# Kernel tuning notes

Hardware: AMD Instinct MI355X
Metric: run time of the kernel (lower is better)

## Reference

```python
import jax, jax.numpy as jnp
import numpy as np

N_ATOMS = 10000
N_EDGES = 160000
N_SPECIES = 8
N_STRUCT = 8
C = 16        # n_element_channels
N_MAX = 4     # radial functions per l
N_BASIS = 8   # bessel basis size
L_MAX = 3
CUTOFF = 5.0
K = N_MAX * C             # equivariant channels per l (k_max_l)
K_TOTAL = (L_MAX + 1) * K  # concatenated invariants


def _sph_harm(u):
    """Real spherical harmonics l=0..3 for unit vectors u [E,3] -> [E,16]."""
    x, y, z = u[:, 0], u[:, 1], u[:, 2]
    x2, y2, z2 = x * x, y * y, z * z
    one = jnp.ones_like(x)
    ys = [
        0.28209479 * one,
        0.48860251 * y, 0.48860251 * z, 0.48860251 * x,
        1.09254843 * x * y, 1.09254843 * y * z,
        0.31539157 * (3.0 * z2 - 1.0),
        1.09254843 * x * z, 0.54627422 * (x2 - y2),
        0.59004359 * y * (3.0 * x2 - y2), 2.89061144 * x * y * z,
        0.45704579 * y * (5.0 * z2 - 1.0), 0.37317633 * z * (5.0 * z2 - 3.0),
        0.45704579 * x * (5.0 * z2 - 1.0), 1.44530572 * z * (x2 - y2),
        0.59004359 * x * (x2 - 3.0 * y2),
    ]
    return jnp.stack(ys, axis=-1)


def _radial(r, W_rad):
    """Bessel radial basis with cosine cutoff, projected per l. r [E] -> [E, L+1, N_MAX]."""
    n = jnp.arange(1, N_BASIS + 1, dtype=r.dtype)
    rr = jnp.maximum(r, 1e-6)
    basis = jnp.sqrt(2.0 / CUTOFF) * jnp.sin(n[None, :] * jnp.pi * rr[:, None] / CUTOFF) / rr[:, None]
    fc = 0.5 * (jnp.cos(jnp.pi * jnp.clip(r / CUTOFF, 0.0, 1.0)) + 1.0)  # smooth cutoff
    return jnp.einsum('eb,lbn->eln', basis * fc[:, None], W_rad)


def _mp_layer(h, senders, receivers, sh, R, W_inv, cemb):
    """One equivariant message-passing + CG(l x l -> 0) invariant contraction."""
    hs = h[senders]  # gather neighbor scalars [E, C]
    invs = []
    for l in range(L_MAX + 1):
        sl = sh[:, l * l:(l + 1) * (l + 1)]  # [E, 2l+1]
        # edge message: sh x radial x neighbor features -> [E, 2l+1, N_MAX*C]
        M = jnp.einsum('em,en,ec->emnc', sl, R[:, l], hs)
        M = M.reshape(M.shape[0], 2 * l + 1, K)
        A = jax.ops.segment_sum(M, receivers, num_segments=N_ATOMS)  # scatter to centers
        # CG l (x) l -> L=0 invariant (real-SH convention)
        invs.append(jnp.einsum('nmk,nmk->nk', A, A) / jnp.sqrt(2.0 * l + 1.0))
    inv = jnp.concatenate(invs, axis=-1)  # [N, K_TOTAL]
    h_new = (inv @ W_inv) * cemb  # center element embedding
    return h_new, inv


def setup_inputs() -> dict:
    key = jax.random.key(0)
    ks = jax.random.split(key, 10)
    positions = jax.random.uniform(ks[0], (N_ATOMS, 3), jnp.float32, 0.0, 3.0)
    senders = jax.random.randint(ks[1], (N_EDGES,), 0, N_ATOMS)
    receivers = jax.random.randint(ks[2], (N_EDGES,), 0, N_ATOMS)
    species = jax.random.randint(ks[3], (N_ATOMS,), 0, N_SPECIES)
    structure_ids = jnp.sort(jax.random.randint(ks[4], (N_ATOMS,), 0, N_STRUCT))
    embed = jax.random.normal(ks[5], (N_SPECIES, C), jnp.float32)
    W_rad = jax.random.normal(ks[6], (L_MAX + 1, N_BASIS, N_MAX), jnp.float32) * 0.3
    W_inv1 = jax.random.normal(ks[7], (K_TOTAL, C), jnp.float32) / np.sqrt(K_TOTAL)
    W_inv2 = jax.random.normal(ks[8], (K_TOTAL, C), jnp.float32) / np.sqrt(K_TOTAL)
    w_out = jax.random.normal(ks[9], (K_TOTAL,), jnp.float32) / np.sqrt(K_TOTAL)
    comp_weights = jnp.zeros((N_SPECIES,), jnp.float32)
    return {"positions": positions, "embed": embed, "W_rad": W_rad,
            "W_inv1": W_inv1, "W_inv2": W_inv2, "w_out": w_out,
            "comp_weights": comp_weights, "senders": senders,
            "receivers": receivers, "species": species,
            "structure_ids": structure_ids}


def reference(positions, embed, W_rad, W_inv1, W_inv2, w_out, comp_weights,
              senders, receivers, species, structure_ids):
    rvec = positions[receivers] - positions[senders]          # [E,3]
    r = jnp.linalg.norm(rvec, axis=-1)
    u = rvec / jnp.maximum(r, 1e-6)[:, None]
    sh = _sph_harm(u)                                          # [E,16]
    R = _radial(r, W_rad)                                      # [E,4,N_MAX]
    cemb = embed[species]                                      # center embedding [N,C]
    h = cemb                                                   # initial features
    h, _ = _mp_layer(h, senders, receivers, sh, R, W_inv1, cemb)
    h, inv2 = _mp_layer(h, senders, receivers, sh, R, W_inv2, cemb)
    e_atom = inv2 @ w_out + comp_weights[species]              # per-atom energies [N]
    return jax.ops.segment_sum(e_atom, structure_ids, num_segments=N_STRUCT)
```

## Files before the change

kernel.cpp:

```cpp
#include <hip/hip_runtime.h>

#define N_ATOMS 10000
#define N_EDGES 160000
#define N_STRUCT 8
#define D_PAD 48
#define EDW 48
#define N_SLOTS (N_ATOMS * D_PAD)
#define B4 4
#define PI_F 3.14159265358979323846f


__global__ void init_kernel(int* __restrict__ cursor, float* __restrict__ accum) {
    int i = blockIdx.x * blockDim.x + threadIdx.x;
    if (i < N_ATOMS) cursor[i] = i * D_PAD;
    if (i < N_STRUCT) accum[i] = 0.f;
}

__global__ void scatter_kernel(const int* __restrict__ receivers, int* __restrict__ cursor,
                               int* __restrict__ perm) {
    int e = blockIdx.x * blockDim.x + threadIdx.x;
    if (e < N_EDGES) perm[e] = atomicAdd(&cursor[receivers[e]], 1);
}

__global__ void pad_kernel(const int* __restrict__ cursor, float* __restrict__ edat) {
    int i = blockIdx.x * blockDim.x + threadIdx.x;
    if (i >= N_ATOMS * 3) return;
    int a = i / 3, j = i % 3;
    int cnt = cursor[a] - a * D_PAD;
    if (cnt > D_PAD) cnt = D_PAD;
    int c4 = (cnt + B4 - 1) / B4 * B4;
    if (c4 > D_PAD) c4 = D_PAD;
    int slot = cnt + j;
    if (slot < c4) {
        float4 z = make_float4(0.f, 0.f, 0.f, 0.f);
        float4* p = (float4*)(edat + (size_t)(a * D_PAD + slot) * EDW);
        #pragma unroll
        for (int k = 0; k < 12; ++k) p[k] = z;
    }
}

__global__ void emb_kernel(const float* __restrict__ embed, const int* __restrict__ species,
                           float* __restrict__ h0) {
    int i = blockIdx.x * blockDim.x + threadIdx.x;
    if (i < N_ATOMS * 16) {
        int a = i >> 4, c = i & 15;
        h0[i] = embed[species[a] * 16 + c];
    }
}

__global__ void gather_hs(const int* __restrict__ snd, const int* __restrict__ cursor,
                          const float* __restrict__ h, float* __restrict__ edat) {
    int slot = blockIdx.x * blockDim.x + threadIdx.x;
    if (slot >= N_SLOTS) return;
    int a = slot / D_PAD, j = slot - a * D_PAD;
    int cnt = cursor[a] - a * D_PAD;
    if (cnt > D_PAD) cnt = D_PAD;
    if (j >= cnt) return;
    int s = snd[slot];
    const float4* hp = (const float4*)(h + (size_t)s * 16);
    float4* ep = (float4*)(edat + (size_t)slot * EDW + 32);
    ep[0] = hp[0]; ep[1] = hp[1]; ep[2] = hp[2]; ep[3] = hp[3];
}

__global__ void transpose_winv(const float* __restrict__ A, const float* __restrict__ B,
                               float* __restrict__ AT, float* __restrict__ BT) {
    int i = blockIdx.x * blockDim.x + threadIdx.x;
    if (i < 4096) {
        int k = i >> 4, c = i & 15;
        AT[c * 256 + k] = A[i];
    } else if (i < 8192) {
        int j = i - 4096;
        int k = j >> 4, c = j & 15;
        BT[c * 256 + k] = B[j];
    }
}


__global__ void edge_geom(const float* __restrict__ pos, const float* __restrict__ W_rad,
                          const int* __restrict__ senders, const int* __restrict__ receivers,
                          const int* __restrict__ perm,
                          float* __restrict__ edat, int* __restrict__ snd) {
    int e = blockIdx.x * blockDim.x + threadIdx.x;
    if (e >= N_EDGES) return;
    int s = senders[e], rc = receivers[e];
    int p = perm[e];
    float dx = pos[rc * 3 + 0] - pos[s * 3 + 0];
    float dy = pos[rc * 3 + 1] - pos[s * 3 + 1];
    float dz = pos[rc * 3 + 2] - pos[s * 3 + 2];
    float r = sqrtf(dx * dx + dy * dy + dz * dz);
    float rr = fmaxf(r, 1e-6f);
    float inv = 1.0f / rr;
    float x = dx * inv, y = dy * inv, z = dz * inv;
    float x2 = x * x, y2 = y * y, z2 = z * z;
    float she[16];
    she[0]  = 0.28209479f;
    she[1]  = 0.48860251f * y;
    she[2]  = 0.48860251f * z;
    she[3]  = 0.48860251f * x;
    she[4]  = 1.09254843f * x * y;
    she[5]  = 1.09254843f * y * z;
    she[6]  = 0.31539157f * (3.0f * z2 - 1.0f);
    she[7]  = 1.09254843f * x * z;
    she[8]  = 0.54627422f * (x2 - y2);
    she[9]  = 0.59004359f * y * (3.0f * x2 - y2);
    she[10] = 2.89061144f * x * y * z;
    she[11] = 0.45704579f * y * (5.0f * z2 - 1.0f);
    she[12] = 0.37317633f * z * (5.0f * z2 - 3.0f);
    she[13] = 0.45704579f * x * (5.0f * z2 - 1.0f);
    she[14] = 1.44530572f * z * (x2 - y2);
    she[15] = 0.59004359f * x * (x2 - 3.0f * y2);
    float* ed = edat + (size_t)p * EDW;
    ((float4*)ed)[0] = make_float4(she[0], she[1], she[2], she[3]);
    ((float4*)ed)[1] = make_float4(she[4], she[5], she[6], she[7]);
    ((float4*)ed)[2] = make_float4(she[8], she[9], she[10], she[11]);
    ((float4*)ed)[3] = make_float4(she[12], she[13], she[14], she[15]);
    float fc = 0.5f * (cosf(PI_F * fminf(r * 0.2f, 1.0f)) + 1.0f);
    const float c0 = 0.6324555320336759f;
    float bfv[8];
    #pragma unroll
    for (int n = 0; n < 8; ++n)
        bfv[n] = c0 * sinf((float)(n + 1) * PI_F * rr * 0.2f) * inv * fc;
    float Re[16];
    #pragma unroll
    for (int l = 0; l < 4; ++l) {
        #pragma unroll
        for (int n = 0; n < 4; ++n) {
            float acc = 0.0f;
            #pragma unroll
            for (int b = 0; b < 8; ++b) acc = fmaf(bfv[b], W_rad[l * 32 + b * 4 + n], acc);
            Re[l * 4 + n] = acc;
        }
    }
    ((float4*)ed)[4] = make_float4(Re[0], Re[1], Re[2], Re[3]);
    ((float4*)ed)[5] = make_float4(Re[4], Re[5], Re[6], Re[7]);
    ((float4*)ed)[6] = make_float4(Re[8], Re[9], Re[10], Re[11]);
    ((float4*)ed)[7] = make_float4(Re[12], Re[13], Re[14], Re[15]);
    snd[p] = s;
}


__global__ __launch_bounds__(64, 7) void mp_accum(
    const float* __restrict__ edat,
    const int* __restrict__ cursor,
    float* __restrict__ Abuf)
{
    const int lane = threadIdx.x;
    const int atom = blockIdx.x;
    const int m = lane >> 2, cg = lane & 3;
    const int l = (m >= 9) ? 3 : (m >= 4) ? 2 : (m >= 1) ? 1 : 0;
    const int l4 = l * 4, cg4 = cg * 4;

    int cnt = cursor[atom] - atom * D_PAD;
    if (cnt > D_PAD) cnt = D_PAD;
    const int nb = (cnt + B4 - 1) / B4;

    const float* strip = edat + (size_t)atom * (D_PAD * EDW);

    float acc[4][4];
    #pragma unroll
    for (int n = 0; n < 4; ++n)
        #pragma unroll
        for (int j = 0; j < 4; ++j) acc[n][j] = 0.f;

    for (int b = 0; b < nb; ++b) {
        const float* bp = strip + b * (B4 * EDW);
        float  shv[B4];
        float4 rv[B4];
        float4 hv[B4];
        #pragma unroll
        for (int q = 0; q < B4; ++q) {
            const float* eq = bp + q * EDW;
            shv[q] = eq[m];
            rv[q]  = *(const float4*)(eq + 16 + l4);
            hv[q]  = *(const float4*)(eq + 32 + cg4);
        }
        #pragma unroll
        for (int q = 0; q < B4; ++q) {
            float hvj[4] = {hv[q].x, hv[q].y, hv[q].z, hv[q].w};
            float rvn[4] = {rv[q].x, rv[q].y, rv[q].z, rv[q].w};
            #pragma unroll
            for (int j = 0; j < 4; ++j) {
                float ww = shv[q] * hvj[j];
                #pragma unroll
                for (int n = 0; n < 4; ++n)
                    acc[n][j] = fmaf(ww, rvn[n], acc[n][j]);
            }
        }
    }

    float* Ap = Abuf + (size_t)atom * 1024 + m * 64 + cg4;
    #pragma unroll
    for (int n = 0; n < 4; ++n)
        *(float4*)&Ap[n * 16] =
            make_float4(acc[n][0], acc[n][1], acc[n][2], acc[n][3]);
}


#define SROW 260

__global__ __launch_bounds__(256, 2) void mp_inv2(
    const float* __restrict__ Abuf,
    const float* __restrict__ W_invT,
    const float* __restrict__ cemb, float* __restrict__ h_out,
    const float* __restrict__ w_out, const float* __restrict__ comp_w,
    const int* __restrict__ species, const int* __restrict__ sids,
    float* __restrict__ accum, int do_energy)
{
    __shared__ __attribute__((aligned(16))) float sWT[16 * SROW];
    __shared__ __attribute__((aligned(16))) float sInv[16 * SROW];
    __shared__ __attribute__((aligned(16))) float sTmp[4][1024];
    __shared__ float sE[16];

    const int t = threadIdx.x;
    const int w = t >> 6, lane = t & 63;
    const int blk = blockIdx.x;

    if (!do_energy) {
        #pragma unroll
        for (int i = 0; i < 16; ++i) {
            int idx = i * 256 + t;
            sWT[(idx >> 8) * SROW + (idx & 255)] = W_invT[idx];
        }
    }

    const float4* A4 = (const float4*)Abuf;
    #pragma unroll
    for (int g = 0; g < 4; ++g) {
        const int atomL = g * 4 + w;
        const int atom = blk * 16 + atomL;
        #pragma unroll
        for (int i = 0; i < 4; ++i) {
            float4 v = A4[(size_t)atom * 256 + i * 64 + lane];
            *(float4*)&sTmp[w][(i * 64 + lane) * 4] =
                make_float4(v.x * v.x, v.y * v.y, v.z * v.z, v.w * v.w);
        }
        const float* T = &sTmp[w][0];
        const int k = lane;
        float s0 = T[k];
        float s1 = T[64 + k] + T[128 + k] + T[192 + k];
        float s2 = T[256 + k] + T[320 + k] + T[384 + k] + T[448 + k] + T[512 + k];
        float s3 = T[576 + k] + T[640 + k] + T[704 + k] + T[768 + k]
                 + T[832 + k] + T[896 + k] + T[960 + k];
        const float i0 = s0;
        const float i1 = s1 * 0.57735026918962576f;
        const float i2 = s2 * 0.44721359549995794f;
        const float i3 = s3 * 0.37796447300922720f;

        if (do_energy) {
            float pe = i0 * w_out[k] + i1 * w_out[64 + k]
                     + i2 * w_out[128 + k] + i3 * w_out[192 + k];
            #pragma unroll
            for (int off = 32; off > 0; off >>= 1) pe += __shfl_down(pe, off);
            if (lane == 0) sE[atomL] = pe;
        } else {
            float* si = &sInv[atomL * SROW];
            si[k] = i0; si[64 + k] = i1; si[128 + k] = i2; si[192 + k] = i3;
        }
    }
    __syncthreads();

    if (do_energy) {
        if (t == 0) {
            const int base = blk * 16;
            int cursid = sids[base];
            float run = 0.f;
            for (int a = 0; a < 16; ++a) {
                int sid = sids[base + a];
                float e = sE[a] + comp_w[species[base + a]];
                if (sid != cursid) { atomicAdd(&accum[cursid], run); run = 0.f; cursid = sid; }
                run += e;
            }
            atomicAdd(&accum[cursid], run);
        }
    } else {
        const int aL = t >> 4, c = t & 15;
        const float* ivp = &sInv[aL * SROW];
        const float* wvp = &sWT[c * SROW];
        float p = 0.f;
        #pragma unroll
        for (int kk = 0; kk < 64; ++kk) {
            float4 iv = *(const float4*)&ivp[kk * 4];
            float4 wv = *(const float4*)&wvp[kk * 4];
            p = fmaf(iv.x, wv.x, p);
            p = fmaf(iv.y, wv.y, p);
            p = fmaf(iv.z, wv.z, p);
            p = fmaf(iv.w, wv.w, p);
        }
        const int gi = blk * 256 + t;
        h_out[gi] = p * cemb[gi];
    }
}

__global__ void out_kernel(const float* __restrict__ accum, float* __restrict__ out) {
    int t = threadIdx.x;
    if (t < N_STRUCT) out[t] = accum[t];
}


extern "C" void kernel_launch(void* const* d_in, const int* in_sizes, int n_in,
                              void* d_out, int out_size, void* d_ws, size_t ws_size,
                              hipStream_t stream) {
    const float* positions = (const float*)d_in[0];
    const float* embed     = (const float*)d_in[1];
    const float* W_rad     = (const float*)d_in[2];
    const float* W_inv1    = (const float*)d_in[3];
    const float* W_inv2    = (const float*)d_in[4];
    const float* w_out     = (const float*)d_in[5];
    const float* comp_w    = (const float*)d_in[6];
    const int* senders    = (const int*)d_in[7];
    const int* receivers  = (const int*)d_in[8];
    const int* species    = (const int*)d_in[9];
    const int* sids       = (const int*)d_in[10];
    float* out = (float*)d_out;

    char* ws = (char*)d_ws;
    size_t off = 0;
    auto alloc = [&](size_t bytes) -> void* {
        void* p = ws + off;
        off = (off + bytes + 255) & ~(size_t)255;
        return p;
    };
    float* edat     = (float*)alloc((size_t)N_SLOTS * EDW * 4);
    float* Abuf     = (float*)alloc((size_t)N_ATOMS * 1024 * 4);
    float* h0       = (float*)alloc((size_t)N_ATOMS * 16 * 4);
    float* h1       = (float*)alloc((size_t)N_ATOMS * 16 * 4);
    int*   cursor   = (int*)alloc((size_t)N_ATOMS * 4);
    int*   perm     = (int*)alloc((size_t)N_EDGES * 4);
    int*   snd      = (int*)alloc((size_t)N_SLOTS * 4);
    float* accum    = (float*)alloc(8 * 4);
    float* WT1      = (float*)alloc(4096 * 4);
    float* WT2      = (float*)alloc(4096 * 4);

    const int EB = (N_EDGES + 255) / 256;
    const int HB = (N_ATOMS * 16 + 255) / 256;
    const int AB = (N_ATOMS + 255) / 256;
    const int PB = (N_ATOMS * 3 + 255) / 256;
    const int SB = (N_SLOTS + 255) / 256;

    init_kernel<<<AB, 256, 0, stream>>>(cursor, accum);
    scatter_kernel<<<EB, 256, 0, stream>>>(receivers, cursor, perm);
    pad_kernel<<<PB, 256, 0, stream>>>(cursor, edat);
    edge_geom<<<EB, 256, 0, stream>>>(positions, W_rad, senders, receivers, perm,
                                      edat, snd);
    emb_kernel<<<HB, 256, 0, stream>>>(embed, species, h0);
    transpose_winv<<<32, 256, 0, stream>>>(W_inv1, W_inv2, WT1, WT2);

    gather_hs<<<SB, 256, 0, stream>>>(snd, cursor, h0, edat);
    mp_accum<<<N_ATOMS, 64, 0, stream>>>(edat, cursor, Abuf);
    mp_inv2<<<N_ATOMS / 16, 256, 0, stream>>>(Abuf, WT1, h0, h1,
                                              w_out, comp_w, species, sids, accum, 0);
    gather_hs<<<SB, 256, 0, stream>>>(snd, cursor, h1, edat);
    mp_accum<<<N_ATOMS, 64, 0, stream>>>(edat, cursor, Abuf);
    mp_inv2<<<N_ATOMS / 16, 256, 0, stream>>>(Abuf, WT2, h0, h1,
                                              w_out, comp_w, species, sids, accum, 1);

    out_kernel<<<1, 64, 0, stream>>>(accum, out);
}
```

Baseline: 184.4 us.

## Fuse neighbor-feature gather and invariant contraction into the accumulation kernel

Drops the separate gather_hs pass that copied sender features into the padded edge buffer. Each wavefront now loads its slot's sender indices once, broadcasts them by shuffle, and reads h directly from the small feature table. The edge record shrinks from 48 to 32 floats, and pad slots get a zero sender index. The squared-norm CG contraction also moves into the accumulation kernel, so only 256 invariants per atom are written instead of the 1024-float A tensor. This cuts global traffic and removes two launches, at the cost of scattered h loads, which should stay mostly in cache.

```diff
diff --git a/kernel.cpp b/kernel.cpp
--- a/kernel.cpp
+++ b/kernel.cpp
@@ -4,10 +4,11 @@
 #define N_EDGES 160000
 #define N_STRUCT 8
 #define D_PAD 48
-#define EDW 48
+#define EDW 32
 #define N_SLOTS (N_ATOMS * D_PAD)
 #define B4 4
 #define PI_F 3.14159265358979323846f
+#define SROW 260
 
 
 __global__ void init_kernel(int* __restrict__ cursor, float* __restrict__ accum) {
@@ -22,7 +23,8 @@
     if (e < N_EDGES) perm[e] = atomicAdd(&cursor[receivers[e]], 1);
 }
 
-__global__ void pad_kernel(const int* __restrict__ cursor, float* __restrict__ edat) {
+__global__ void pad_kernel(const int* __restrict__ cursor, float* __restrict__ edat,
+                           int* __restrict__ snd) {
     int i = blockIdx.x * blockDim.x + threadIdx.x;
     if (i >= N_ATOMS * 3) return;
     int a = i / 3, j = i % 3;
@@ -35,7 +37,8 @@
         float4 z = make_float4(0.f, 0.f, 0.f, 0.f);
         float4* p = (float4*)(edat + (size_t)(a * D_PAD + slot) * EDW);
         #pragma unroll
-        for (int k = 0; k < 12; ++k) p[k] = z;
+        for (int k = 0; k < 8; ++k) p[k] = z;
+        snd[a * D_PAD + slot] = 0;
     }
 }
 
@@ -46,20 +49,6 @@
         int a = i >> 4, c = i & 15;
         h0[i] = embed[species[a] * 16 + c];
     }
-}
-
-__global__ void gather_hs(const int* __restrict__ snd, const int* __restrict__ cursor,
-                          const float* __restrict__ h, float* __restrict__ edat) {
-    int slot = blockIdx.x * blockDim.x + threadIdx.x;
-    if (slot >= N_SLOTS) return;
-    int a = slot / D_PAD, j = slot - a * D_PAD;
-    int cnt = cursor[a] - a * D_PAD;
-    if (cnt > D_PAD) cnt = D_PAD;
-    if (j >= cnt) return;
-    int s = snd[slot];
-    const float4* hp = (const float4*)(h + (size_t)s * 16);
-    float4* ep = (float4*)(edat + (size_t)slot * EDW + 32);
-    ep[0] = hp[0]; ep[1] = hp[1]; ep[2] = hp[2]; ep[3] = hp[3];
 }
 
 __global__ void transpose_winv(const float* __restrict__ A, const float* __restrict__ B,
@@ -139,11 +128,12 @@
 }
 
 
-__global__ __launch_bounds__(64, 7) void mp_accum(
-    const float* __restrict__ edat,
-    const int* __restrict__ cursor,
-    float* __restrict__ Abuf)
+__global__ __launch_bounds__(64, 7) void mp_accum2(
+    const float* __restrict__ edat, const int* __restrict__ snd,
+    const int* __restrict__ cursor, const float* __restrict__ h_in,
+    float* __restrict__ Inv)
 {
+    __shared__ __attribute__((aligned(16))) float wl[1024];
     const int lane = threadIdx.x;
     const int atom = blockIdx.x;
     const int m = lane >> 2, cg = lane & 3;
@@ -154,6 +144,9 @@
     if (cnt > D_PAD) cnt = D_PAD;
     const int nb = (cnt + B4 - 1) / B4;
 
+    int sv = 0;
+    if (lane < D_PAD) sv = snd[atom * D_PAD + lane];
+
     const float* strip = edat + (size_t)atom * (D_PAD * EDW);
 
     float acc[4][4];
@@ -163,7 +156,8 @@
         for (int j = 0; j < 4; ++j) acc[n][j] = 0.f;
 
     for (int b = 0; b < nb; ++b) {
-        const float* bp = strip + b * (B4 * EDW);
+        const int s0 = b * B4;
+        const float* bp = strip + s0 * EDW;
         float  shv[B4];
         float4 rv[B4];
         float4 hv[B4];
@@ -172,7 +166,7 @@
             const float* eq = bp + q * EDW;
             shv[q] = eq[m];
             rv[q]  = *(const float4*)(eq + 16 + l4);
-            hv[q]  = *(const float4*)(eq + 32 + cg4);
+            hv[q]  = *(const float4*)(h_in + (size_t)__shfl(sv, s0 + q) * 16 + cg4);
         }
         #pragma unroll
         for (int q = 0; q < B4; ++q) {
@@ -188,18 +182,29 @@
         }
     }
 
-    float* Ap = Abuf + (size_t)atom * 1024 + m * 64 + cg4;
     #pragma unroll
     for (int n = 0; n < 4; ++n)
-        *(float4*)&Ap[n * 16] =
-            make_float4(acc[n][0], acc[n][1], acc[n][2], acc[n][3]);
-}
-
-
-#define SROW 260
-
-__global__ __launch_bounds__(256, 2) void mp_inv2(
-    const float* __restrict__ Abuf,
+        *(float4*)&wl[m * 64 + n * 16 + cg4] =
+            make_float4(acc[n][0] * acc[n][0], acc[n][1] * acc[n][1],
+                        acc[n][2] * acc[n][2], acc[n][3] * acc[n][3]);
+
+    const float* T = wl;
+    const int k = lane;
+    float s0v = T[k];
+    float s1v = T[64 + k] + T[128 + k] + T[192 + k];
+    float s2v = T[256 + k] + T[320 + k] + T[384 + k] + T[448 + k] + T[512 + k];
+    float s3v = T[576 + k] + T[640 + k] + T[704 + k] + T[768 + k]
+              + T[832 + k] + T[896 + k] + T[960 + k];
+    float* ip = Inv + (size_t)atom * 256;
+    ip[k]       = s0v;
+    ip[64 + k]  = s1v * 0.57735026918962576f;
+    ip[128 + k] = s2v * 0.44721359549995794f;
+    ip[192 + k] = s3v * 0.37796447300922720f;
+}
+
+
+__global__ __launch_bounds__(256, 2) void mp_inv3(
+    const float* __restrict__ Inv,
     const float* __restrict__ W_invT,
     const float* __restrict__ cemb, float* __restrict__ h_out,
     const float* __restrict__ w_out, const float* __restrict__ comp_w,
@@ -208,58 +213,27 @@
 {
     __shared__ __attribute__((aligned(16))) float sWT[16 * SROW];
     __shared__ __attribute__((aligned(16))) float sInv[16 * SROW];
-    __shared__ __attribute__((aligned(16))) float sTmp[4][1024];
     __shared__ float sE[16];
-
     const int t = threadIdx.x;
     const int w = t >> 6, lane = t & 63;
     const int blk = blockIdx.x;
 
-    if (!do_energy) {
-        #pragma unroll
-        for (int i = 0; i < 16; ++i) {
-            int idx = i * 256 + t;
-            sWT[(idx >> 8) * SROW + (idx & 255)] = W_invT[idx];
-        }
-    }
-
-    const float4* A4 = (const float4*)Abuf;
-    #pragma unroll
-    for (int g = 0; g < 4; ++g) {
-        const int atomL = g * 4 + w;
-        const int atom = blk * 16 + atomL;
-        #pragma unroll
-        for (int i = 0; i < 4; ++i) {
-            float4 v = A4[(size_t)atom * 256 + i * 64 + lane];
-            *(float4*)&sTmp[w][(i * 64 + lane) * 4] =
-                make_float4(v.x * v.x, v.y * v.y, v.z * v.z, v.w * v.w);
-        }
-        const float* T = &sTmp[w][0];
-        const int k = lane;
-        float s0 = T[k];
-        float s1 = T[64 + k] + T[128 + k] + T[192 + k];
-        float s2 = T[256 + k] + T[320 + k] + T[384 + k] + T[448 + k] + T[512 + k];
-        float s3 = T[576 + k] + T[640 + k] + T[704 + k] + T[768 + k]
-                 + T[832 + k] + T[896 + k] + T[960 + k];
-        const float i0 = s0;
-        const float i1 = s1 * 0.57735026918962576f;
-        const float i2 = s2 * 0.44721359549995794f;
-        const float i3 = s3 * 0.37796447300922720f;
-
-        if (do_energy) {
-            float pe = i0 * w_out[k] + i1 * w_out[64 + k]
-                     + i2 * w_out[128 + k] + i3 * w_out[192 + k];
+    if (do_energy) {
+        #pragma unroll
+        for (int g = 0; g < 4; ++g) {
+            const int atomL = g * 4 + w;
+            const size_t base = (size_t)(blk * 16 + atomL) * 256;
+            float i0 = Inv[base + lane];
+            float i1 = Inv[base + 64 + lane];
+            float i2 = Inv[base + 128 + lane];
+            float i3 = Inv[base + 192 + lane];
+            float pe = i0 * w_out[lane] + i1 * w_out[64 + lane]
+                     + i2 * w_out[128 + lane] + i3 * w_out[192 + lane];
             #pragma unroll
             for (int off = 32; off > 0; off >>= 1) pe += __shfl_down(pe, off);
             if (lane == 0) sE[atomL] = pe;
-        } else {
-            float* si = &sInv[atomL * SROW];
-            si[k] = i0; si[64 + k] = i1; si[128 + k] = i2; si[192 + k] = i3;
-        }
-    }
-    __syncthreads();
-
-    if (do_energy) {
+        }
+        __syncthreads();
         if (t == 0) {
             const int base = blk * 16;
             int cursid = sids[base];
@@ -273,6 +247,14 @@
             atomicAdd(&accum[cursid], run);
         }
     } else {
+        #pragma unroll
+        for (int i = 0; i < 16; ++i) {
+            int idx = i * 256 + t;
+            int row = idx >> 8, col = idx & 255;
+            sWT[row * SROW + col]  = W_invT[idx];
+            sInv[row * SROW + col] = Inv[(size_t)blk * 4096 + idx];
+        }
+        __syncthreads();
         const int aL = t >> 4, c = t & 15;
         const float* ivp = &sInv[aL * SROW];
         const float* wvp = &sWT[c * SROW];
@@ -321,7 +303,7 @@
         return p;
     };
     float* edat     = (float*)alloc((size_t)N_SLOTS * EDW * 4);
-    float* Abuf     = (float*)alloc((size_t)N_ATOMS * 1024 * 4);
+    float* Inv      = (float*)alloc((size_t)N_ATOMS * 256 * 4);
     float* h0       = (float*)alloc((size_t)N_ATOMS * 16 * 4);
     float* h1       = (float*)alloc((size_t)N_ATOMS * 16 * 4);
     int*   cursor   = (int*)alloc((size_t)N_ATOMS * 4);
@@ -335,23 +317,20 @@
     const int HB = (N_ATOMS * 16 + 255) / 256;
     const int AB = (N_ATOMS + 255) / 256;
     const int PB = (N_ATOMS * 3 + 255) / 256;
-    const int SB = (N_SLOTS + 255) / 256;
 
     init_kernel<<<AB, 256, 0, stream>>>(cursor, accum);
     scatter_kernel<<<EB, 256, 0, stream>>>(receivers, cursor, perm);
-    pad_kernel<<<PB, 256, 0, stream>>>(cursor, edat);
+    pad_kernel<<<PB, 256, 0, stream>>>(cursor, edat, snd);
     edge_geom<<<EB, 256, 0, stream>>>(positions, W_rad, senders, receivers, perm,
                                       edat, snd);
     emb_kernel<<<HB, 256, 0, stream>>>(embed, species, h0);
     transpose_winv<<<32, 256, 0, stream>>>(W_inv1, W_inv2, WT1, WT2);
 
-    gather_hs<<<SB, 256, 0, stream>>>(snd, cursor, h0, edat);
-    mp_accum<<<N_ATOMS, 64, 0, stream>>>(edat, cursor, Abuf);
-    mp_inv2<<<N_ATOMS / 16, 256, 0, stream>>>(Abuf, WT1, h0, h1,
+    mp_accum2<<<N_ATOMS, 64, 0, stream>>>(edat, snd, cursor, h0, Inv);
+    mp_inv3<<<N_ATOMS / 16, 256, 0, stream>>>(Inv, WT1, h0, h1,
                                               w_out, comp_w, species, sids, accum, 0);
-    gather_hs<<<SB, 256, 0, stream>>>(snd, cursor, h1, edat);
-    mp_accum<<<N_ATOMS, 64, 0, stream>>>(edat, cursor, Abuf);
-    mp_inv2<<<N_ATOMS / 16, 256, 0, stream>>>(Abuf, WT2, h0, h1,
+    mp_accum2<<<N_ATOMS, 64, 0, stream>>>(edat, snd, cursor, h1, Inv);
+    mp_inv3<<<N_ATOMS / 16, 256, 0, stream>>>(Inv, WT2, h0, h1,
                                               w_out, comp_w, species, sids, accum, 1);
 
     out_kernel<<<1, 64, 0, stream>>>(accum, out);
```

Result: faster. 161.8 us (-12.2%).
